# Optimization experiments

Hardware: AMD Instinct MI355X
Metric: run time of the kernel (lower is better)

The kernel has to match this reference:

```python
import jax, jax.numpy as jnp
import numpy as np

GAMMA = 12.0
P_NORM = 1

NUM_ENT = 500000
NUM_REL = 500
D = 256
B = 500000


def setup_inputs() -> dict:
    key = jax.random.key(0)
    k1, k2, k3 = jax.random.split(key, 3)
    node_embeddings = jax.random.normal(k1, (NUM_ENT, D), dtype=jnp.float32)
    rel_embeddings = jax.random.normal(k2, (NUM_REL, D), dtype=jnp.float32)
    # all indices < NUM_REL so col 1 is a valid relation index and cols 0/2 valid entity indices
    triplets = jax.random.randint(k3, (B, 3), 0, NUM_REL, dtype=jnp.int64)
    return {
        "node_embeddings": node_embeddings,
        "rel_embeddings": rel_embeddings,
        "triplets": triplets,
    }


def reference(node_embeddings, rel_embeddings, triplets):
    h = node_embeddings[triplets[:, 0]]  # [B, D]
    r = rel_embeddings[triplets[:, 1]]   # [B, D]
    t = node_embeddings[triplets[:, 2]]  # [B, D]
    diff = h + r - t
    if P_NORM == 1:
        dist = jnp.sum(jnp.abs(diff), axis=-1)
    else:
        dist = jnp.sqrt(jnp.sum(diff * diff, axis=-1))
    return GAMMA - dist  # [B]
```

## Files before the change

kernel.cpp:

```cpp
#include <hip/hip_runtime.h>

#define GAMMA 12.0f
#define DIM 256
#define NROWS 500
#define CW 64
#define NCHUNK 4
#define ROWS_PAD 504
#define REGION_HALVES (ROWS_PAD * CW)
#define REGION_BYTES (REGION_HALVES * 2)
#define THREADS 1024
#define WAVES 16
#define PASSES 16
#define TPB 2048

typedef _Float16 h2 __attribute__((ext_vector_type(2)));

static __device__ __forceinline__ unsigned short f2h(float x) {
    _Float16 h = (_Float16)x;
    return __builtin_bit_cast(unsigned short, h);
}

static __device__ __forceinline__ float acc_pair(unsigned uh, unsigned ur, unsigned ut, float acc) {
    h2 h = __builtin_bit_cast(h2, uh);
    h2 r = __builtin_bit_cast(h2, ur);
    h2 t = __builtin_bit_cast(h2, ut);
    h2 d = (h + r) - t;
    unsigned ad = __builtin_bit_cast(unsigned, d) & 0x7FFF7FFFu;
    h2 one = { (_Float16)1.0f, (_Float16)1.0f };
    return __builtin_amdgcn_fdot2(__builtin_bit_cast(h2, ad), one, acc, false);
}

__global__ __launch_bounds__(256) void transe_convert(
    const float* __restrict__ node, const float* __restrict__ rel,
    unsigned short* __restrict__ out)
{
    const int per = NROWS * DIM;
    int t8 = (blockIdx.x * 256 + threadIdx.x) * 8;
    if (t8 >= 2 * per) return;
    int table = t8 >= per;
    int e = t8 - table * per;
    const float* src = table ? rel : node;
    float4 f0 = *(const float4*)(src + e);
    float4 f1 = *(const float4*)(src + e + 4);
    int row = e >> 8;
    int d = e & (DIM - 1);
    int c = d >> 6, w = d & (CW - 1);
    union { unsigned short us[8]; uint4 v; } o;
    o.us[0] = f2h(f0.x); o.us[1] = f2h(f0.y); o.us[2] = f2h(f0.z); o.us[3] = f2h(f0.w);
    o.us[4] = f2h(f1.x); o.us[5] = f2h(f1.y); o.us[6] = f2h(f1.z); o.us[7] = f2h(f1.w);
    *(uint4*)(out + (size_t)(table * NCHUNK + c) * REGION_HALVES + row * CW + w) = o.v;
}

__global__ __launch_bounds__(THREADS) void transe_main(
    const unsigned short* __restrict__ tab16,
    const int* __restrict__ trip,
    const float* __restrict__ node_f32,
    const float* __restrict__ rel_f32,
    float* __restrict__ out, int B)
{
    __shared__ __align__(16) unsigned short ltab[2 * REGION_HALVES];
    __shared__ int ltrip[TPB];

    const int tid  = threadIdx.x;
    const int wid  = tid >> 6;
    const int lane = tid & 63;
    const int g    = lane >> 3;
    const int m    = lane & 7;
    const int moff = m * 16;
    const long base = (long)blockIdx.x * TPB;

    const char* srcb = (const char*)tab16;
    char* ldsb = (char*)ltab;

    #pragma unroll 1
    for (int i = wid; i < 126; i += WAVES) {
        int region = i >= 63;
        int k = region ? (i - 63) : i;
        const char* src = srcb + (size_t)(region * NCHUNK + 0) * REGION_BYTES
                        + (size_t)k * 1024 + (size_t)lane * 16;
        char* dst = ldsb + region * REGION_BYTES + k * 1024;
        __builtin_amdgcn_global_load_lds(
            (const __attribute__((address_space(1))) unsigned int*)src,
            (__attribute__((address_space(3))) unsigned int*)dst, 16, 0, 0);
    }

    for (int s = tid; s < TPB; s += THREADS) {
        long j = base + s;
        unsigned pk;
        if (j < B) {
            int h = trip[3 * j], r = trip[3 * j + 1], t = trip[3 * j + 2];
            unsigned oob = ((unsigned)h >= NROWS || (unsigned)r >= NROWS || (unsigned)t >= NROWS)
                           ? (1u << 30) : 0u;
            unsigned hc = (unsigned)min(max(h, 0), NROWS - 1);
            unsigned rc = (unsigned)min(max(r, 0), NROWS - 1);
            unsigned tc = (unsigned)min(max(t, 0), NROWS - 1);
            pk = hc | (rc << 10) | (tc << 20) | oob;
        } else pk = 1u << 31;
        ltrip[s] = (int)pk;
    }
    __syncthreads();

    unsigned pidx[PASSES];
    #pragma unroll
    for (int p = 0; p < PASSES; ++p)
        pidx[p] = (unsigned)ltrip[wid * (8 * PASSES) + p * 8 + g];

    float acc[PASSES];
    #pragma unroll
    for (int p = 0; p < PASSES; ++p) acc[p] = 0.f;

    for (int c = 0; c < NCHUNK; ++c) {
        if (c) {
            __syncthreads();
            #pragma unroll 1
            for (int i = wid; i < 126; i += WAVES) {
                int region = i >= 63;
                int k = region ? (i - 63) : i;
                const char* src = srcb + (size_t)(region * NCHUNK + c) * REGION_BYTES
                                + (size_t)k * 1024 + (size_t)lane * 16;
                char* dst = ldsb + region * REGION_BYTES + k * 1024;
                __builtin_amdgcn_global_load_lds(
                    (const __attribute__((address_space(1))) unsigned int*)src,
                    (__attribute__((address_space(3))) unsigned int*)dst, 16, 0, 0);
            }
            __syncthreads();
        }

        #pragma unroll
        for (int p = 0; p < PASSES; ++p) {
            unsigned pk = pidx[p];
            unsigned hb = (pk & 1023u) << 7;
            unsigned rb = ((pk >> 10) & 1023u) << 7;
            unsigned tb = ((pk >> 20) & 1023u) << 7;
            uint4 hv = *(const uint4*)(ldsb + hb + moff);
            uint4 rv = *(const uint4*)(ldsb + REGION_BYTES + rb + moff);
            uint4 tv = *(const uint4*)(ldsb + tb + moff);
            float a = acc[p];
            a = acc_pair(hv.x, rv.x, tv.x, a);
            a = acc_pair(hv.y, rv.y, tv.y, a);
            a = acc_pair(hv.z, rv.z, tv.z, a);
            a = acc_pair(hv.w, rv.w, tv.w, a);
            acc[p] = a;
        }
    }

    #pragma unroll
    for (int p = 0; p < PASSES; ++p) {
        float a = acc[p];
        a += __shfl_xor(a, 1, 64);
        a += __shfl_xor(a, 2, 64);
        a += __shfl_xor(a, 4, 64);
        if (m == 0) {
            unsigned pk = pidx[p];
            int slot = wid * (8 * PASSES) + p * 8 + g;
            long j = base + slot;
            if (!(pk >> 30)) {
                out[j] = GAMMA - a;
            } else if (!(pk >> 31)) {
                int hh = trip[3 * j], rr = trip[3 * j + 1], tt = trip[3 * j + 2];
                float s = 0.f;
                for (int d = 0; d < DIM; ++d)
                    s += fabsf(node_f32[(size_t)hh * DIM + d] + rel_f32[(size_t)rr * DIM + d]
                             - node_f32[(size_t)tt * DIM + d]);
                out[j] = GAMMA - s;
            }
        }
    }
}

__global__ __launch_bounds__(256) void transe_direct(
    const float* __restrict__ node_emb,
    const float* __restrict__ rel_emb,
    const int*   __restrict__ triplets,
    float*       __restrict__ out, int B)
{
    const int wave = blockIdx.x * (blockDim.x >> 6) + (threadIdx.x >> 6);
    const int lane = threadIdx.x & 63;
    if (wave >= B) return;
    const int h_idx = triplets[wave * 3 + 0];
    const int r_idx = triplets[wave * 3 + 1];
    const int t_idx = triplets[wave * 3 + 2];
    const float4 h = ((const float4*)(node_emb + (size_t)h_idx * DIM))[lane];
    const float4 r = ((const float4*)(rel_emb  + (size_t)r_idx * DIM))[lane];
    const float4 t = ((const float4*)(node_emb + (size_t)t_idx * DIM))[lane];
    float s = fabsf(h.x + r.x - t.x) + fabsf(h.y + r.y - t.y)
            + fabsf(h.z + r.z - t.z) + fabsf(h.w + r.w - t.w);
    #pragma unroll
    for (int off = 32; off > 0; off >>= 1) s += __shfl_down(s, off, 64);
    if (lane == 0) out[wave] = GAMMA - s;
}

extern "C" void kernel_launch(void* const* d_in, const int* in_sizes, int n_in,
                              void* d_out, int out_size, void* d_ws, size_t ws_size,
                              hipStream_t stream) {
    const float* node_emb = (const float*)d_in[0];
    const float* rel_emb  = (const float*)d_in[1];
    const int*   triplets = (const int*)d_in[2];
    float*       out      = (float*)d_out;
    const int B = out_size;

    const size_t ws_needed = (size_t)2 * NCHUNK * REGION_HALVES * sizeof(unsigned short);
    if (ws_size < ws_needed) {
        const int grid = (B + 3) / 4;
        transe_direct<<<grid, 256, 0, stream>>>(node_emb, rel_emb, triplets, out, B);
        return;
    }

    unsigned short* tab16 = (unsigned short*)d_ws;

    const int conv_threads = 2 * NROWS * DIM / 8;
    transe_convert<<<(conv_threads + 255) / 256, 256, 0, stream>>>(node_emb, rel_emb, tab16);

    const int grid = (B + TPB - 1) / TPB;
    transe_main<<<grid, THREADS, 0, stream>>>(tab16, triplets, node_emb, rel_emb, out, B);
}
```

Baseline: 30.81 us.

## Double-buffer node chunks in LDS and read relation rows from global

The LDS buffer now holds two node-embedding chunks instead of one node chunk plus one relation chunk. The next chunk is prefetched with global_load_lds while the current one is being computed, and a single barrier per chunk replaces the previous pair. Relation rows are now read directly from the fp16 global table, with a one-pass-ahead register prefetch. This is meant to hide the staging latency behind compute, at the cost of cache-served global loads for relation rows and reliance on the barrier to wait for the asynchronous LDS loads.

```diff
diff --git a/kernel.cpp b/kernel.cpp
--- a/kernel.cpp
+++ b/kernel.cpp
@@ -8,6 +8,7 @@
 #define ROWS_PAD 504
 #define REGION_HALVES (ROWS_PAD * CW)
 #define REGION_BYTES (REGION_HALVES * 2)
+#define STAGE_ITERS (REGION_BYTES / 1024)
 #define THREADS 1024
 #define WAVES 16
 #define PASSES 16
@@ -58,7 +59,7 @@
     const float* __restrict__ rel_f32,
     float* __restrict__ out, int B)
 {
-    __shared__ __align__(16) unsigned short ltab[2 * REGION_HALVES];
+    __shared__ __align__(16) unsigned short lbuf[2 * REGION_HALVES];
     __shared__ int ltrip[TPB];
 
     const int tid  = threadIdx.x;
@@ -70,15 +71,12 @@
     const long base = (long)blockIdx.x * TPB;
 
     const char* srcb = (const char*)tab16;
-    char* ldsb = (char*)ltab;
+    char* ldsb = (char*)lbuf;
 
     #pragma unroll 1
-    for (int i = wid; i < 126; i += WAVES) {
-        int region = i >= 63;
-        int k = region ? (i - 63) : i;
-        const char* src = srcb + (size_t)(region * NCHUNK + 0) * REGION_BYTES
-                        + (size_t)k * 1024 + (size_t)lane * 16;
-        char* dst = ldsb + region * REGION_BYTES + k * 1024;
+    for (int i = wid; i < STAGE_ITERS; i += WAVES) {
+        const char* src = srcb + (size_t)i * 1024 + (size_t)lane * 16;
+        char* dst = ldsb + i * 1024;
         __builtin_amdgcn_global_load_lds(
             (const __attribute__((address_space(1))) unsigned int*)src,
             (__attribute__((address_space(3))) unsigned int*)dst, 16, 0, 0);
@@ -110,31 +108,31 @@
     for (int p = 0; p < PASSES; ++p) acc[p] = 0.f;
 
     for (int c = 0; c < NCHUNK; ++c) {
-        if (c) {
-            __syncthreads();
+        if (c + 1 < NCHUNK) {
+            const char* cb = srcb + (size_t)(c + 1) * REGION_BYTES;
+            char* db = ldsb + ((c + 1) & 1) * REGION_BYTES;
             #pragma unroll 1
-            for (int i = wid; i < 126; i += WAVES) {
-                int region = i >= 63;
-                int k = region ? (i - 63) : i;
-                const char* src = srcb + (size_t)(region * NCHUNK + c) * REGION_BYTES
-                                + (size_t)k * 1024 + (size_t)lane * 16;
-                char* dst = ldsb + region * REGION_BYTES + k * 1024;
+            for (int i = wid; i < STAGE_ITERS; i += WAVES) {
                 __builtin_amdgcn_global_load_lds(
-                    (const __attribute__((address_space(1))) unsigned int*)src,
-                    (__attribute__((address_space(3))) unsigned int*)dst, 16, 0, 0);
+                    (const __attribute__((address_space(1))) unsigned int*)
+                        (cb + (size_t)i * 1024 + (size_t)lane * 16),
+                    (__attribute__((address_space(3))) unsigned int*)(db + i * 1024),
+                    16, 0, 0);
             }
-            __syncthreads();
         }
 
+        const char* lbase = ldsb + (c & 1) * REGION_BYTES;
+        const char* relc  = srcb + (size_t)(NCHUNK + c) * REGION_BYTES;
+
+        uint4 rnext = *(const uint4*)(relc + (((pidx[0] >> 10) & 1023u) << 7) + moff);
         #pragma unroll
         for (int p = 0; p < PASSES; ++p) {
+            uint4 rv = rnext;
+            if (p + 1 < PASSES)
+                rnext = *(const uint4*)(relc + (((pidx[p + 1] >> 10) & 1023u) << 7) + moff);
             unsigned pk = pidx[p];
-            unsigned hb = (pk & 1023u) << 7;
-            unsigned rb = ((pk >> 10) & 1023u) << 7;
-            unsigned tb = ((pk >> 20) & 1023u) << 7;
-            uint4 hv = *(const uint4*)(ldsb + hb + moff);
-            uint4 rv = *(const uint4*)(ldsb + REGION_BYTES + rb + moff);
-            uint4 tv = *(const uint4*)(ldsb + tb + moff);
+            uint4 hv = *(const uint4*)(lbase + ((pk & 1023u) << 7) + moff);
+            uint4 tv = *(const uint4*)(lbase + (((pk >> 20) & 1023u) << 7) + moff);
             float a = acc[p];
             a = acc_pair(hv.x, rv.x, tv.x, a);
             a = acc_pair(hv.y, rv.y, tv.y, a);
@@ -142,6 +140,8 @@
             a = acc_pair(hv.w, rv.w, tv.w, a);
             acc[p] = a;
         }
+
+        __syncthreads();
     }
 
     #pragma unroll
```

After: 28.68 us, median of 2. 6.9% less time.
